# Performance work log

Measured on AMD Instinct MI355X. Metric: run time of the kernel, lower is better.

Reference implementation:

```python
import math
import jax, jax.numpy as jnp
import numpy as np

B, T, H, E, K, F = 4, 4096, 512, 8, 2, 2048
CAP_FACTOR, ROUND_TO = 0.3125, 128


def _capacity(num_tokens):
    cap = math.ceil(CAP_FACTOR * num_tokens)
    cap = ROUND_TO * math.ceil(cap / ROUND_TO)
    return max(1, min(cap, num_tokens))


def setup_inputs() -> dict:
    key = jax.random.key(0)
    k0, k1, k2, k3 = jax.random.split(key, 4)
    x = jax.random.normal(k0, (B, T, H), jnp.float32)
    router_w = jax.random.normal(k1, (H, E), jnp.float32) * 0.02
    w1 = jax.random.normal(k2, (E, H, F), jnp.float32) * (1.0 / np.sqrt(H))
    b1 = jnp.zeros((E, F), jnp.float32)
    w2 = jax.random.normal(k3, (E, F, H), jnp.float32) * (1.0 / np.sqrt(F))
    b2 = jnp.zeros((E, H), jnp.float32)
    return {"x": x, "router_w": router_w, "w1": w1, "b1": b1, "w2": w2, "b2": b2}


def reference(x, router_w, w1, b1, w2, b2):
    Bc, Tc, Hc = x.shape
    n = Bc * Tc
    cap = _capacity(n)  # static: 5120
    flat = x.reshape(n, Hc)

    # Router + top-k selection (fp32 logits, softmax over selected logits)
    logits = (flat @ router_w).astype(jnp.float32)          # [n, E]
    sel_logits, expert_idx = jax.lax.top_k(logits, K)       # [n, K]
    weights = jax.nn.softmax(sel_logits, axis=-1)           # [n, K]

    # Flatten (token, k) assignments and sort by expert (stable)
    fe = expert_idx.reshape(-1).astype(jnp.int32)           # [n*K]
    fw = weights.reshape(-1)
    tok = jnp.broadcast_to(jnp.arange(n, dtype=jnp.int32)[:, None], expert_idx.shape).reshape(-1)
    order = jnp.argsort(fe)  # jax sort is stable
    se, st, sw = fe[order], tok[order], fw[order]

    # Per-expert slot index; assignments beyond capacity are dropped
    counts = jnp.bincount(se, length=E)                     # [E]
    offsets = (jnp.cumsum(counts) - counts).astype(jnp.int32)
    slot = jnp.arange(se.shape[0], dtype=jnp.int32) - offsets[se]
    keep = slot < cap
    sw = jnp.where(keep, sw, 0.0)                           # dropped tokens contribute 0

    # Pack into fixed-capacity expert buffers (out-of-range slots dropped)
    sx = flat[st]                                           # [n*K, H]
    expert_inputs = jnp.zeros((E, cap, Hc), flat.dtype).at[se, slot].set(sx, mode='drop')

    # Grouped expert MLP: Dense(F) -> GELU -> Dense(H)
    h = jax.nn.gelu(jnp.einsum('ech,ehf->ecf', expert_inputs, w1) + b1[:, None, :])
    out = jnp.einsum('ecf,efh->ech', h, w2) + b2[:, None, :]

    # Zero invalid (unused) slots
    clipped = jnp.minimum(counts, cap)
    valid = (jnp.arange(cap, dtype=jnp.int32)[None, :] < clipped[:, None])[..., None]
    out = jnp.where(valid, out, 0)

    # Scatter-combine weighted expert outputs back to tokens
    slot_c = jnp.minimum(slot, cap - 1)                     # dropped rows have weight 0
    gathered = out[se, slot_c] * sw[:, None].astype(out.dtype)
    combined = jnp.zeros((n, Hc), out.dtype).at[st].add(gathered)
    return combined.reshape(Bc, Tc, Hc)
```

## Files before the change

kernel.cpp:

```cpp
#include <hip/hip_runtime.h>
#include <hip/hip_bf16.h>

#define NTOK 16384
#define HD   512
#define ED   8
#define FD   2048
#define CAP  5120
#define NA   32768

typedef __bf16 bf16x8 __attribute__((ext_vector_type(8)));
typedef float  f32x4  __attribute__((ext_vector_type(4)));

static constexpr size_t OFF_EIDX = 0;
static constexpr size_t OFF_WGT  = 131072;
static constexpr size_t OFF_STOK = 262144;
static constexpr size_t OFF_ASLOT= 425984;
static constexpr size_t OFF_ECNT = 557056;
static constexpr size_t OFF_W2T  = 1u << 20;
static constexpr size_t OFF_H    = OFF_W2T + (size_t)ED*HD*FD*2;
static constexpr size_t OFF_W1T  = OFF_H   + (size_t)ED*CAP*FD*2;
static constexpr size_t OFF_XBF  = OFF_W1T + (size_t)ED*FD*HD*2;
static constexpr size_t OFF_EOUT = OFF_XBF + (size_t)NTOK*HD*2;

__device__ __forceinline__ unsigned short f2bf(float f) {
    __bf16 b = (__bf16)f;
    return __builtin_bit_cast(unsigned short, b);
}
__device__ __forceinline__ unsigned short f2h(float f) {
    _Float16 h = (_Float16)f;
    return __builtin_bit_cast(unsigned short, h);
}
__device__ __forceinline__ float h2f(unsigned short u) {
    return (float)__builtin_bit_cast(_Float16, u);
}

__device__ __forceinline__ float gelu_fast(float v) {
    const float t = v * v;
    const float u = v * fmaf(t, 0.0713548214f, 1.5957691216f);
    const float e = __expf(-u);
    return v * __builtin_amdgcn_rcpf(1.f + e);
}

__device__ __forceinline__ void gl16(const unsigned short* g, unsigned short* l) {
    __builtin_amdgcn_global_load_lds(
        (const __attribute__((address_space(1))) unsigned int*)(const void*)g,
        (__attribute__((address_space(3))) unsigned int*)(void*)l, 16, 0, 0);
}

__global__ __launch_bounds__(256) void transpose_cast_kernel(
    const float* __restrict__ in, unsigned short* __restrict__ out, int R, int C)
{
    __shared__ unsigned short tile[32][33];
    const int e = blockIdx.z;
    in  += (size_t)e * R * C;
    out += (size_t)e * R * C;
    const int r0 = blockIdx.y * 32, c0 = blockIdx.x * 32;
    const int tr = threadIdx.x >> 3, tc = (threadIdx.x & 7) * 4;
    const float4 v = *(const float4*)(in + (size_t)(r0 + tr) * C + c0 + tc);
    tile[tr][tc + 0] = f2bf(v.x);
    tile[tr][tc + 1] = f2bf(v.y);
    tile[tr][tc + 2] = f2bf(v.z);
    tile[tr][tc + 3] = f2bf(v.w);
    __syncthreads();
    ushort4 o;
    o.x = tile[tc + 0][tr]; o.y = tile[tc + 1][tr];
    o.z = tile[tc + 2][tr]; o.w = tile[tc + 3][tr];
    *(ushort4*)(out + (size_t)(c0 + tr) * R + r0 + tc) = o;
}

__global__ __launch_bounds__(256) void router_kernel(
    const float* __restrict__ x, const float* __restrict__ rw,
    int* __restrict__ eidx, float* __restrict__ wgt,
    unsigned short* __restrict__ xbf)
{
    __shared__ float rws[HD * ED];
    const int tid = threadIdx.x;
    for (int i = tid * 4; i < HD * ED; i += 256 * 4)
        *(float4*)(rws + i) = *(const float4*)(rw + i);
    __syncthreads();

    const int wid = tid >> 6, lane = tid & 63;
    const int t = blockIdx.x * 4 + wid;
    const float* xr = x + (size_t)t * HD;

    float acc[ED];
#pragma unroll
    for (int e = 0; e < ED; e++) acc[e] = 0.f;

    float4 xv0 = *(const float4*)(xr + lane * 8);
    float4 xv1 = *(const float4*)(xr + lane * 8 + 4);
    float xv[8] = {xv0.x, xv0.y, xv0.z, xv0.w, xv1.x, xv1.y, xv1.z, xv1.w};

    union { unsigned short us[8]; uint4 v; } pk;
#pragma unroll
    for (int j = 0; j < 8; j++) pk.us[j] = f2bf(xv[j]);
    *(uint4*)(xbf + (size_t)t * HD + lane * 8) = pk.v;

#pragma unroll
    for (int j = 0; j < 8; j++) {
        const int h = lane * 8 + j;
#pragma unroll
        for (int e = 0; e < ED; e++) acc[e] += xv[j] * rws[h * ED + e];
    }
#pragma unroll
    for (int off = 32; off >= 1; off >>= 1) {
#pragma unroll
        for (int e = 0; e < ED; e++) acc[e] += __shfl_down(acc[e], off);
    }
    if (lane == 0) {
        int e0 = 0; float l0 = acc[0];
        for (int e = 1; e < ED; e++) if (acc[e] > l0) { l0 = acc[e]; e0 = e; }
        int e1 = 0; float l1 = -1e30f;
        for (int e = 0; e < ED; e++) {
            if (e == e0) continue;
            if (acc[e] > l1) { l1 = acc[e]; e1 = e; }
        }
        const float ex = expf(l1 - l0);
        const float inv = 1.f / (1.f + ex);
        eidx[t * 2 + 0] = e0;  eidx[t * 2 + 1] = e1;
        wgt [t * 2 + 0] = inv; wgt [t * 2 + 1] = ex * inv;
    }
}

__global__ __launch_bounds__(1024) void scan_kernel(
    const int* __restrict__ eidx,
    int* __restrict__ stok, int* __restrict__ aslot, int* __restrict__ ecnt)
{
    __shared__ int running[ED];
    __shared__ int wcnt[16][ED];
    const int tid = threadIdx.x;

    for (int i = tid; i < ED * CAP; i += 1024) stok[i] = -1;
    if (tid < ED) running[tid] = 0;
    __syncthreads();

    const int lane = tid & 63, wid = tid >> 6;
    const unsigned long long below = (1ull << lane) - 1ull;

    for (int c = 0; c < NA / 1024; c++) {
        const int a = c * 1024 + tid;
        const int e = eidx[a];
        int myrank = 0;
#pragma unroll
        for (int ee = 0; ee < ED; ee++) {
            unsigned long long m = __ballot(e == ee);
            if (ee == e) myrank = __popcll(m & below);
            if (lane == 0) wcnt[wid][ee] = __popcll(m);
        }
        __syncthreads();
        int woff = 0;
        for (int ww = 0; ww < wid; ww++) woff += wcnt[ww][e];
        const int slot = running[e] + woff + myrank;
        if (slot < CAP) {
            stok[e * CAP + slot] = a >> 1;
            aslot[a] = slot;
        } else {
            aslot[a] = -1;
        }
        __syncthreads();
        if (tid < ED) {
            int tot = 0;
            for (int ww = 0; ww < 16; ww++) tot += wcnt[ww][tid];
            running[tid] += tot;
        }
        __syncthreads();
    }
    if (tid < ED) ecnt[tid] = running[tid] < CAP ? running[tid] : CAP;
}

template<int KD, int ND, int NT, bool G1>
__global__ __launch_bounds__(256) void gemm_mfma(
    const unsigned short* __restrict__ Abase,
    const unsigned short* __restrict__ Bt,
    const float* __restrict__ bias,
    const int* __restrict__ stok,
    const int* __restrict__ ecnt,
    unsigned short* __restrict__ hout)
{
    constexpr int BUFE = 128 * 32;
    __shared__ __align__(16) unsigned short As[2 * BUFE];
    __shared__ __align__(16) unsigned short Bs[2 * BUFE];

    const int tid = threadIdx.x;
    const int e  = blockIdx.x & 7;
    const int g  = blockIdx.x >> 3;
    const int n0 = (g % NT) * 128;
    const int m0 = (g / NT) * 128;

    if (m0 >= ecnt[e]) return;

    const int lane = tid & 63;
    const int wid  = tid >> 6;

    const int rsub = lane >> 2;
    const int csw  = (lane & 3) ^ ((rsub >> 1) & 3);

    const unsigned short *ag0, *ag1, *bg0, *bg1;
    {
        const int R0 = (wid * 2 + 0) * 16 + rsub;
        const int R1 = (wid * 2 + 1) * 16 + rsub;
        size_t a0, a1;
        if constexpr (G1) {
            const int t0 = stok[e * CAP + m0 + R0];
            const int t1 = stok[e * CAP + m0 + R1];
            a0 = (size_t)(t0 >= 0 ? t0 : 0);
            a1 = (size_t)(t1 >= 0 ? t1 : 0);
        } else {
            a0 = (size_t)(e * CAP + m0 + R0);
            a1 = (size_t)(e * CAP + m0 + R1);
        }
        ag0 = Abase + a0 * KD + csw * 8;
        ag1 = Abase + a1 * KD + csw * 8;
        bg0 = Bt + ((size_t)e * ND + n0 + R0) * KD + csw * 8;
        bg1 = Bt + ((size_t)e * ND + n0 + R1) * KD + csw * 8;
    }
    unsigned short* lA = As + (wid * 2) * 512;
    unsigned short* lB = Bs + (wid * 2) * 512;

    const int wrow = (wid & 1) * 64;
    const int wcol = (wid >> 1) * 64;
    const int l15  = lane & 15;
    const int quad = lane >> 4;
    const int xq   = quad ^ ((l15 >> 1) & 3);
    const int fA   = (wrow + l15) * 32 + xq * 8;
    const int fB   = (wcol + l15) * 32 + xq * 8;

    f32x4 acc[4][4];
#pragma unroll
    for (int i = 0; i < 4; i++)
#pragma unroll
        for (int j = 0; j < 4; j++) acc[i][j] = (f32x4)0.f;

#define STAGE(B, KC)                                                           \
    {                                                                          \
        gl16(ag0 + (KC), lA + (B) * BUFE);                                     \
        gl16(ag1 + (KC), lA + (B) * BUFE + 512);                               \
        gl16(bg0 + (KC), lB + (B) * BUFE);                                     \
        gl16(bg1 + (KC), lB + (B) * BUFE + 512);                               \
    }

#define COMPUTE(B)                                                             \
    {                                                                          \
        const unsigned short* Ab = As + (B) * BUFE;                            \
        const unsigned short* Bb = Bs + (B) * BUFE;                            \
        bf16x8 af[4], bfv[4];                                                  \
        _Pragma("unroll")                                                      \
        for (int i = 0; i < 4; i++) af[i]  = *(const bf16x8*)(Ab + fA + i * 512); \
        _Pragma("unroll")                                                      \
        for (int j = 0; j < 4; j++) bfv[j] = *(const bf16x8*)(Bb + fB + j * 512); \
        _Pragma("unroll")                                                      \
        for (int i = 0; i < 4; i++)                                            \
            _Pragma("unroll")                                                  \
            for (int j = 0; j < 4; j++)                                        \
                acc[i][j] = __builtin_amdgcn_mfma_f32_16x16x32_bf16(           \
                    bfv[j], af[i], acc[i][j], 0, 0, 0);                        \
    }

    STAGE(0, 0);
    __syncthreads();

    for (int kc = 0; kc <= KD - 128; kc += 64) {
        STAGE(1, kc + 32);
        COMPUTE(0);
        __syncthreads();
        STAGE(0, kc + 64);
        COMPUTE(1);
        __syncthreads();
    }
    STAGE(1, KD - 32);
    COMPUTE(0);
    __syncthreads();
    COMPUTE(1);
#undef STAGE
#undef COMPUTE

#pragma unroll
    for (int i = 0; i < 4; i++) {
        unsigned short* hrow = hout
            + ((size_t)e * CAP + m0 + wrow + i * 16 + l15) * ND
            + n0 + wcol + quad * 4;
#pragma unroll
        for (int j = 0; j < 4; j++) {
            const float4 b4 = *(const float4*)(
                bias + (size_t)e * ND + n0 + wcol + j * 16 + quad * 4);
            const float v0 = acc[i][j][0] + b4.x;
            const float v1 = acc[i][j][1] + b4.y;
            const float v2 = acc[i][j][2] + b4.z;
            const float v3 = acc[i][j][3] + b4.w;
            ushort4 o;
            if constexpr (G1) {
                o.x = f2bf(gelu_fast(v0)); o.y = f2bf(gelu_fast(v1));
                o.z = f2bf(gelu_fast(v2)); o.w = f2bf(gelu_fast(v3));
            } else {
                o.x = f2h(v0); o.y = f2h(v1); o.z = f2h(v2); o.w = f2h(v3);
            }
            *(ushort4*)(hrow + j * 16) = o;
        }
    }
}

__global__ __launch_bounds__(256) void combine_kernel(
    const unsigned short* __restrict__ eout,
    const int* __restrict__ eidx, const int* __restrict__ aslot,
    const float* __restrict__ wgt, float* __restrict__ out)
{
    const int tid = threadIdx.x;
    const int t  = blockIdx.x * 2 + (tid >> 7);
    const int h0 = (tid & 127) * 4;
    float r0 = 0.f, r1 = 0.f, r2 = 0.f, r3 = 0.f;
#pragma unroll
    for (int k = 0; k < 2; k++) {
        const int a = t * 2 + k;
        const int s = aslot[a];
        if (s >= 0) {
            const float w = wgt[a];
            const int e = eidx[a];
            const ushort4 v = *(const ushort4*)(eout + ((size_t)e * CAP + s) * HD + h0);
            r0 += w * h2f(v.x); r1 += w * h2f(v.y);
            r2 += w * h2f(v.z); r3 += w * h2f(v.w);
        }
    }
    float4 o; o.x = r0; o.y = r1; o.z = r2; o.w = r3;
    *(float4*)(out + (size_t)t * HD + h0) = o;
}

extern "C" void kernel_launch(void* const* d_in, const int* in_sizes, int n_in,
                              void* d_out, int out_size, void* d_ws, size_t ws_size,
                              hipStream_t stream)
{
    const float* x  = (const float*)d_in[0];
    const float* rw = (const float*)d_in[1];
    const float* w1 = (const float*)d_in[2];
    const float* b1 = (const float*)d_in[3];
    const float* w2 = (const float*)d_in[4];
    const float* b2 = (const float*)d_in[5];
    float* out = (float*)d_out;

    char* ws = (char*)d_ws;
    int*   eidx  = (int*)  (ws + OFF_EIDX);
    float* wgt   = (float*)(ws + OFF_WGT);
    int*   stok  = (int*)  (ws + OFF_STOK);
    int*   aslot = (int*)  (ws + OFF_ASLOT);
    int*   ecnt  = (int*)  (ws + OFF_ECNT);
    unsigned short* w2t  = (unsigned short*)(ws + OFF_W2T);
    unsigned short* hbuf = (unsigned short*)(ws + OFF_H);
    unsigned short* w1t  = (unsigned short*)(ws + OFF_W1T);
    unsigned short* xbf  = (unsigned short*)(ws + OFF_XBF);
    unsigned short* eout = (unsigned short*)(ws + OFF_EOUT);

    transpose_cast_kernel<<<dim3(FD / 32, HD / 32, ED), 256, 0, stream>>>(w1, w1t, HD, FD);
    transpose_cast_kernel<<<dim3(HD / 32, FD / 32, ED), 256, 0, stream>>>(w2, w2t, FD, HD);
    router_kernel<<<NTOK / 4, 256, 0, stream>>>(x, rw, eidx, wgt, xbf);
    scan_kernel<<<1, 1024, 0, stream>>>(eidx, stok, aslot, ecnt);

    gemm_mfma<HD, FD, FD/128, true>
        <<<8 * (FD/128) * (CAP/128), 256, 0, stream>>>(
        xbf, w1t, b1, stok, ecnt, hbuf);

    gemm_mfma<FD, HD, HD/128, false>
        <<<8 * (HD/128) * (CAP/128), 256, 0, stream>>>(
        hbuf, w2t, b2, nullptr, ecnt, eout);

    combine_kernel<<<NTOK / 2, 256, 0, stream>>>(eout, eidx, aslot, wgt, out);
}
```

Baseline: 464.6 us.

## Parallelize routing scan and switch GEMM staging to register-prefetched LDS writes

The scan kernel now counts each chunk's per-wave expert histogram up front, builds the offsets with a wave-level prefix scan per expert, and then assigns slots without a chain of per-chunk barriers. The GEMM drops direct global-to-LDS loads in favour of register prefetch: the next K-slab is loaded into registers, written to the alternate LDS buffer, and a custom lgkmcnt wait plus barrier is used. The scan change removes serialized syncthreads overhead. The GEMM change trades the async direct-to-LDS path for more VGPR pressure and explicit LDS stores.

Measured after the change: 456.3 us. No clear change (-1.8%).

```diff
diff --git a/kernel.cpp b/kernel.cpp
--- a/kernel.cpp
+++ b/kernel.cpp
@@ -39,12 +39,6 @@
     const float u = v * fmaf(t, 0.0713548214f, 1.5957691216f);
     const float e = __expf(-u);
     return v * __builtin_amdgcn_rcpf(1.f + e);
-}
-
-__device__ __forceinline__ void gl16(const unsigned short* g, unsigned short* l) {
-    __builtin_amdgcn_global_load_lds(
-        (const __attribute__((address_space(1))) unsigned int*)(const void*)g,
-        (__attribute__((address_space(3))) unsigned int*)(void*)l, 16, 0, 0);
 }
 
 __global__ __launch_bounds__(256) void transpose_cast_kernel(
@@ -126,16 +120,43 @@
     const int* __restrict__ eidx,
     int* __restrict__ stok, int* __restrict__ aslot, int* __restrict__ ecnt)
 {
-    __shared__ int running[ED];
-    __shared__ int wcnt[16][ED];
+    __shared__ int wcnt[32][16][ED];
+    __shared__ int woff[32][16][ED];
     const int tid = threadIdx.x;
-
-    for (int i = tid; i < ED * CAP; i += 1024) stok[i] = -1;
-    if (tid < ED) running[tid] = 0;
-    __syncthreads();
-
     const int lane = tid & 63, wid = tid >> 6;
     const unsigned long long below = (1ull << lane) - 1ull;
+
+    for (int i = tid; i < ED * CAP; i += 1024) stok[i] = -1;
+
+    for (int c = 0; c < NA / 1024; c++) {
+        const int e = eidx[c * 1024 + tid];
+#pragma unroll
+        for (int ee = 0; ee < ED; ee++) {
+            unsigned long long m = __ballot(e == ee);
+            if (lane == 0) wcnt[c][wid][ee] = __popcll(m);
+        }
+    }
+    __syncthreads();
+
+    if (wid < ED) {
+        const int e = wid;
+        int carry = 0;
+#pragma unroll
+        for (int r = 0; r < 8; r++) {
+            const int idx = r * 64 + lane;
+            const int v = wcnt[idx >> 4][idx & 15][e];
+            int s = v;
+#pragma unroll
+            for (int off = 1; off < 64; off <<= 1) {
+                int u = __shfl_up(s, off);
+                if (lane >= off) s += u;
+            }
+            woff[idx >> 4][idx & 15][e] = carry + s - v;
+            carry += __shfl(s, 63);
+        }
+        if (lane == 0) ecnt[e] = carry < CAP ? carry : CAP;
+    }
+    __syncthreads();
 
     for (int c = 0; c < NA / 1024; c++) {
         const int a = c * 1024 + tid;
@@ -145,27 +166,15 @@
         for (int ee = 0; ee < ED; ee++) {
             unsigned long long m = __ballot(e == ee);
             if (ee == e) myrank = __popcll(m & below);
-            if (lane == 0) wcnt[wid][ee] = __popcll(m);
-        }
-        __syncthreads();
-        int woff = 0;
-        for (int ww = 0; ww < wid; ww++) woff += wcnt[ww][e];
-        const int slot = running[e] + woff + myrank;
+        }
+        const int slot = woff[c][wid][e] + myrank;
         if (slot < CAP) {
             stok[e * CAP + slot] = a >> 1;
             aslot[a] = slot;
         } else {
             aslot[a] = -1;
         }
-        __syncthreads();
-        if (tid < ED) {
-            int tot = 0;
-            for (int ww = 0; ww < 16; ww++) tot += wcnt[ww][tid];
-            running[tid] += tot;
-        }
-        __syncthreads();
-    }
-    if (tid < ED) ecnt[tid] = running[tid] < CAP ? running[tid] : CAP;
+    }
 }
 
 template<int KD, int ND, int NT, bool G1>
@@ -192,30 +201,28 @@
     const int lane = tid & 63;
     const int wid  = tid >> 6;
 
-    const int rsub = lane >> 2;
-    const int csw  = (lane & 3) ^ ((rsub >> 1) & 3);
-
-    const unsigned short *ag0, *ag1, *bg0, *bg1;
-    {
-        const int R0 = (wid * 2 + 0) * 16 + rsub;
-        const int R1 = (wid * 2 + 1) * 16 + rsub;
-        size_t a0, a1;
-        if constexpr (G1) {
-            const int t0 = stok[e * CAP + m0 + R0];
-            const int t1 = stok[e * CAP + m0 + R1];
-            a0 = (size_t)(t0 >= 0 ? t0 : 0);
-            a1 = (size_t)(t1 >= 0 ? t1 : 0);
-        } else {
-            a0 = (size_t)(e * CAP + m0 + R0);
-            a1 = (size_t)(e * CAP + m0 + R1);
-        }
-        ag0 = Abase + a0 * KD + csw * 8;
-        ag1 = Abase + a1 * KD + csw * 8;
-        bg0 = Bt + ((size_t)e * ND + n0 + R0) * KD + csw * 8;
-        bg1 = Bt + ((size_t)e * ND + n0 + R1) * KD + csw * 8;
-    }
-    unsigned short* lA = As + (wid * 2) * 512;
-    unsigned short* lB = Bs + (wid * 2) * 512;
+    const int q  = tid & 3;
+    const int r1 = tid >> 2;
+    const int r2 = r1 + 64;
+
+    size_t ai1, ai2;
+    if constexpr (G1) {
+        const int t1 = stok[e * CAP + m0 + r1];
+        const int t2 = stok[e * CAP + m0 + r2];
+        ai1 = (size_t)(t1 >= 0 ? t1 : 0);
+        ai2 = (size_t)(t2 >= 0 ? t2 : 0);
+    } else {
+        ai1 = (size_t)(e * CAP + m0 + r1);
+        ai2 = (size_t)(e * CAP + m0 + r2);
+    }
+    const unsigned short* arow1 = Abase + ai1 * KD + q * 8;
+    const unsigned short* arow2 = Abase + ai2 * KD + q * 8;
+    const unsigned short* brow1 = Bt + ((size_t)e * ND + n0 + r1) * KD + q * 8;
+    const unsigned short* brow2 = Bt + ((size_t)e * ND + n0 + r2) * KD + q * 8;
+
+    const int cSw = q ^ ((r1 >> 1) & 3);
+    const int oW1 = r1 * 32 + cSw * 8;
+    const int oW2 = r2 * 32 + cSw * 8;
 
     const int wrow = (wid & 1) * 64;
     const int wcol = (wid >> 1) * 64;
@@ -231,18 +238,10 @@
 #pragma unroll
         for (int j = 0; j < 4; j++) acc[i][j] = (f32x4)0.f;
 
-#define STAGE(B, KC)                                                           \
+#define COMPUTE(PBUF)                                                          \
     {                                                                          \
-        gl16(ag0 + (KC), lA + (B) * BUFE);                                     \
-        gl16(ag1 + (KC), lA + (B) * BUFE + 512);                               \
-        gl16(bg0 + (KC), lB + (B) * BUFE);                                     \
-        gl16(bg1 + (KC), lB + (B) * BUFE + 512);                               \
-    }
-
-#define COMPUTE(B)                                                             \
-    {                                                                          \
-        const unsigned short* Ab = As + (B) * BUFE;                            \
-        const unsigned short* Bb = Bs + (B) * BUFE;                            \
+        const unsigned short* Ab = As + (PBUF) * BUFE;                         \
+        const unsigned short* Bb = Bs + (PBUF) * BUFE;                         \
         bf16x8 af[4], bfv[4];                                                  \
         _Pragma("unroll")                                                      \
         for (int i = 0; i < 4; i++) af[i]  = *(const bf16x8*)(Ab + fA + i * 512); \
@@ -256,23 +255,45 @@
                     bfv[j], af[i], acc[i][j], 0, 0, 0);                        \
     }
 
-    STAGE(0, 0);
-    __syncthreads();
-
-    for (int kc = 0; kc <= KD - 128; kc += 64) {
-        STAGE(1, kc + 32);
-        COMPUTE(0);
-        __syncthreads();
-        STAGE(0, kc + 64);
-        COMPUTE(1);
-        __syncthreads();
-    }
-    STAGE(1, KD - 32);
-    COMPUTE(0);
-    __syncthreads();
-    COMPUTE(1);
-#undef STAGE
+#define LBAR asm volatile("s_waitcnt lgkmcnt(0)\n\ts_barrier" ::: "memory")
+
+    float4 ra1 = *(const float4*)(arow1);
+    float4 ra2 = *(const float4*)(arow2);
+    float4 rb1 = *(const float4*)(brow1);
+    float4 rb2 = *(const float4*)(brow2);
+    *(float4*)(&As[oW1]) = ra1;
+    *(float4*)(&As[oW2]) = ra2;
+    *(float4*)(&Bs[oW1]) = rb1;
+    *(float4*)(&Bs[oW2]) = rb2;
+    if (32 < KD) {
+        ra1 = *(const float4*)(arow1 + 32);
+        ra2 = *(const float4*)(arow2 + 32);
+        rb1 = *(const float4*)(brow1 + 32);
+        rb2 = *(const float4*)(brow2 + 32);
+    }
+    LBAR;
+
+    int rbuf = 0;
+    for (int kc = 0; kc < KD; kc += 32) {
+        const int wb = (rbuf ^ 1) * BUFE;
+        if (kc + 32 < KD) {
+            *(float4*)(&As[wb + oW1]) = ra1;
+            *(float4*)(&As[wb + oW2]) = ra2;
+            *(float4*)(&Bs[wb + oW1]) = rb1;
+            *(float4*)(&Bs[wb + oW2]) = rb2;
+            if (kc + 64 < KD) {
+                ra1 = *(const float4*)(arow1 + kc + 64);
+                ra2 = *(const float4*)(arow2 + kc + 64);
+                rb1 = *(const float4*)(brow1 + kc + 64);
+                rb2 = *(const float4*)(brow2 + kc + 64);
+            }
+        }
+        COMPUTE(rbuf);
+        LBAR;
+        rbuf ^= 1;
+    }
 #undef COMPUTE
+#undef LBAR
 
 #pragma unroll
     for (int i = 0; i < 4; i++) {
```
